# Optimization experiments

Measured on AMD Instinct MI355X. Metric: run time of the kernel, lower is better.

## Reference

```python
import jax, jax.numpy as jnp
import numpy as np

B, T, N_EMBD, N_HEAD = 2, 2048, 1024, 16
HEAD = N_EMBD // N_HEAD
WINDOW = 64


def setup_inputs() -> dict:
    key = jax.random.key(0)
    kq, kk, kv, kw = jax.random.split(key, 4)
    q = jax.random.normal(kq, (B, T, N_EMBD), dtype=jnp.float32)
    k = jax.random.normal(kk, (B, T, N_EMBD), dtype=jnp.float32)
    v = jax.random.normal(kv, (B, T, N_EMBD), dtype=jnp.float32)
    W_proj = jax.random.normal(kw, (N_EMBD, N_EMBD), dtype=jnp.float32) * (1.0 / np.sqrt(N_EMBD))
    b_proj = jnp.zeros((N_EMBD,), dtype=jnp.float32)
    return {"q": q, "k": k, "v": v, "W_proj": W_proj, "b_proj": b_proj}


def reference(q, k, v, W_proj, b_proj):
    Bsz, Tlen, _ = q.shape
    # split heads: [B, H, T, D]
    qh = q.reshape(Bsz, Tlen, N_HEAD, HEAD).transpose(0, 2, 1, 3)
    kh = k.reshape(Bsz, Tlen, N_HEAD, HEAD).transpose(0, 2, 1, 3)
    vh = v.reshape(Bsz, Tlen, N_HEAD, HEAD).transpose(0, 2, 1, 3)

    scale = 1.0 / np.sqrt(HEAD)
    scores = jnp.einsum('bhqd,bhkd->bhqk', qh, kh) * scale  # [B,H,T,T]

    # windowed additive mask: positions with |i-j| > WINDOW get -inf
    idx = jnp.arange(Tlen)
    dist = jnp.abs(idx[None, :] - idx[:, None])  # [T, T]
    scores = jnp.where(dist[None, None] > WINDOW, -jnp.inf, scores)

    attn = jax.nn.softmax(scores, axis=-1)
    y = jnp.einsum('bhqk,bhkd->bhqd', attn, vh)  # [B,H,T,D]
    y = y.transpose(0, 2, 1, 3).reshape(Bsz, Tlen, N_EMBD)
    return y @ W_proj.T + b_proj
```

## Files before the change

kernel.cpp:

```cpp
#include <hip/hip_runtime.h>
#include <hip/hip_bf16.h>

#define B_SZ 2
#define T_SZ 2048
#define NE   1024
#define NH   16
#define HD   64
#define WIN  64
#define QT   64
#define KT   192
#define GM   4096
#define GN   1024
#define GK   1024
#define KPAD 72
#define VPAD 200

__device__ ushort Wb_static[GN * GK];

__device__ __forceinline__ uint pack2(float lo, float hi) {
    uint r;
    asm("v_cvt_pk_bf16_f32 %0, %1, %2" : "=v"(r) : "v"(lo), "v"(hi));
    return r;
}
__device__ __forceinline__ uint4 pack8(float4 a, float4 b) {
    return make_uint4(pack2(a.x, a.y), pack2(a.z, a.w),
                      pack2(b.x, b.y), pack2(b.z, b.w));
}

typedef __attribute__((ext_vector_type(8))) short frag_ab;
typedef __attribute__((ext_vector_type(4))) float frag_cd;
union FragU { frag_ab f; uint u[4]; };

__global__ __launch_bounds__(256, 3) void attn_mfma_kernel(
    const float* __restrict__ q, const float* __restrict__ k,
    const float* __restrict__ v, const float* __restrict__ W,
    ushort* __restrict__ y)
{
    __shared__ __attribute__((aligned(16))) ushort pool[KT * KPAD + HD * VPAD];
    ushort* Ks = pool;
    ushort* Vt = pool + KT * KPAD;
    ushort* Ps = pool;

    const int bid = blockIdx.x;
    const int swz = ((bid & 7) << 7) | (bid >> 3);
    const int qs  = (swz & 31) * QT;
    const int h   = (swz >> 5) & 15;
    const int b   = swz >> 9;
    const int t   = threadIdx.x;
    const int kstart = qs - WIN;

    const int wv   = t >> 6;
    const int L    = t & 63;
    const int r16  = L & 15;
    const int quad = L >> 4;

    float4 qf0, qf1, qg0, qg1;
    {
        const float* qrow = q + ((size_t)(b * T_SZ + qs + wv * 16 + r16)) * NE + h * HD;
        const float4* p0 = (const float4*)(qrow + quad * 8);
        const float4* p1 = (const float4*)(qrow + 32 + quad * 8);
        qf0 = p0[0]; qf1 = p0[1]; qg0 = p1[0]; qg1 = p1[1];
    }

    {
        const int idx = bid * 256 + t;
        const float4 f = ((const float4*)W)[idx];
        ((uint2*)Wb_static)[idx] = make_uint2(pack2(f.x, f.y), pack2(f.z, f.w));
    }

#pragma unroll
    for (int i = 0; i < 6; ++i) {
        const int c  = t + 256 * i;
        const int j  = c >> 3;
        const int cc = c & 7;
        const int d8 = cc * 8;
        const int jg = kstart + j;
        const int jc = min(max(jg, 0), T_SZ - 1);
        const size_t off = ((size_t)(b * T_SZ + jc)) * NE + h * HD + d8;
        const float4* kp = (const float4*)(k + off);
        const float4* vp = (const float4*)(v + off);
        const float4 k0 = kp[0], k1 = kp[1];
        const float4 v0 = vp[0], v1 = vp[1];
        *(uint4*)&Ks[j * KPAD + d8] = pack8(k0, k1);
        ushort* vtc = &Vt[d8 * VPAD + (((j >> 3) ^ cc) * 8 + (j & 7))];
        const uint p01 = pack2(v0.x, v0.y);
        const uint p23 = pack2(v0.z, v0.w);
        const uint p45 = pack2(v1.x, v1.y);
        const uint p67 = pack2(v1.z, v1.w);
        vtc[0 * VPAD] = (ushort)p01; vtc[1 * VPAD] = (ushort)(p01 >> 16);
        vtc[2 * VPAD] = (ushort)p23; vtc[3 * VPAD] = (ushort)(p23 >> 16);
        vtc[4 * VPAD] = (ushort)p45; vtc[5 * VPAD] = (ushort)(p45 >> 16);
        vtc[6 * VPAD] = (ushort)p67; vtc[7 * VPAD] = (ushort)(p67 >> 16);
    }

    const float QSC = 0.125f * 1.44269504f;
    frag_ab aq0, aq1;
    {
        FragU u0, u1;
        u0.u[0] = pack2(qf0.x * QSC, qf0.y * QSC);
        u0.u[1] = pack2(qf0.z * QSC, qf0.w * QSC);
        u0.u[2] = pack2(qf1.x * QSC, qf1.y * QSC);
        u0.u[3] = pack2(qf1.z * QSC, qf1.w * QSC);
        u1.u[0] = pack2(qg0.x * QSC, qg0.y * QSC);
        u1.u[1] = pack2(qg0.z * QSC, qg0.w * QSC);
        u1.u[2] = pack2(qg1.x * QSC, qg1.y * QSC);
        u1.u[3] = pack2(qg1.z * QSC, qg1.w * QSC);
        aq0 = u0.f; aq1 = u1.f;
    }
    __syncthreads();

    frag_cd sacc[12];
#pragma unroll
    for (int nb = 0; nb < 12; ++nb) sacc[nb] = (frag_cd){0,0,0,0};
    __builtin_amdgcn_s_setprio(1);
#pragma unroll
    for (int nb = 0; nb < 12; ++nb) {
        const frag_ab b0 = *(const frag_ab*)&Ks[(nb * 16 + r16) * KPAD + quad * 8];
        const frag_ab b1 = *(const frag_ab*)&Ks[(nb * 16 + r16) * KPAD + 32 + quad * 8];
        sacc[nb] = __builtin_amdgcn_mfma_f32_16x16x32_bf16(aq0, b0, sacc[nb], 0, 0, 0);
        sacc[nb] = __builtin_amdgcn_mfma_f32_16x16x32_bf16(aq1, b1, sacc[nb], 0, 0, 0);
    }
    __builtin_amdgcn_s_setprio(0);

    const int base_m = wv * 16 + quad * 4;
    float l[4] = {0.f, 0.f, 0.f, 0.f};
#pragma unroll
    for (int nb = 0; nb < 12; ++nb) {
        const int jl = nb * 16 + r16;
        const int jg = kstart + jl;
        const bool jg_ok = (jg >= 0) & (jg < T_SZ);
#pragma unroll
        for (int r = 0; r < 4; ++r) {
            const int mrow = base_m + r;
            const bool valid = jg_ok & ((uint)(jl - mrow) <= 2u * WIN);
            const float p = valid ? exp2f(sacc[nb][r]) : 0.0f;
            l[r] += p;
            sacc[nb][r] = p;
        }
    }
#pragma unroll
    for (int r = 0; r < 4; ++r) {
        l[r] += __shfl_xor(l[r], 1);
        l[r] += __shfl_xor(l[r], 2);
        l[r] += __shfl_xor(l[r], 4);
        l[r] += __shfl_xor(l[r], 8);
    }

    __syncthreads();
#pragma unroll
    for (int nb = 0; nb < 12; ++nb) {
        const int jl = nb * 16 + r16;
        const uint p01 = pack2(sacc[nb][0], sacc[nb][1]);
        const uint p23 = pack2(sacc[nb][2], sacc[nb][3]);
        Ps[(base_m + 0) * VPAD + jl] = (ushort)p01;
        Ps[(base_m + 1) * VPAD + jl] = (ushort)(p01 >> 16);
        Ps[(base_m + 2) * VPAD + jl] = (ushort)p23;
        Ps[(base_m + 3) * VPAD + jl] = (ushort)(p23 >> 16);
    }
    __syncthreads();

    frag_ab ap[6];
#pragma unroll
    for (int kb = 0; kb < 6; ++kb)
        ap[kb] = *(const frag_ab*)&Ps[(wv * 16 + r16) * VPAD + kb * 32 + quad * 8];

    frag_cd oacc[4];
#pragma unroll
    for (int nb = 0; nb < 4; ++nb) oacc[nb] = (frag_cd){0,0,0,0};
    __builtin_amdgcn_s_setprio(1);
#pragma unroll
    for (int nb = 0; nb < 4; ++nb) {
        const int dr  = nb * 16 + r16;
        const int dsw = (dr >> 3) & 7;
#pragma unroll
        for (int kb = 0; kb < 6; ++kb) {
            const frag_ab bv = *(const frag_ab*)&Vt[dr * VPAD + (((kb * 4 + quad) ^ dsw) * 8)];
            oacc[nb] = __builtin_amdgcn_mfma_f32_16x16x32_bf16(ap[kb], bv, oacc[nb], 0, 0, 0);
        }
    }
    __builtin_amdgcn_s_setprio(0);

    float inv[4];
#pragma unroll
    for (int r = 0; r < 4; ++r) inv[r] = 1.0f / l[r];
#pragma unroll
    for (int nb = 0; nb < 4; ++nb) {
        const int d  = nb * 16 + r16;
        const uint p01 = pack2(oacc[nb][0] * inv[0], oacc[nb][1] * inv[1]);
        const uint p23 = pack2(oacc[nb][2] * inv[2], oacc[nb][3] * inv[3]);
        const size_t rb = (size_t)(b * T_SZ + qs + base_m) * NE + h * HD + d;
        y[rb + 0 * NE] = (ushort)p01;
        y[rb + 1 * NE] = (ushort)(p01 >> 16);
        y[rb + 2 * NE] = (ushort)p23;
        y[rb + 3 * NE] = (ushort)(p23 >> 16);
    }
}

__global__ __launch_bounds__(256, 2) void proj_gemm_kernel(
    const ushort* __restrict__ A,
    const float* __restrict__ bias, float* __restrict__ C)
{
    __shared__ __attribute__((aligned(16))) ushort As[128 * 128];
    __shared__ __attribute__((aligned(16))) ushort Bs[64 * 128];

    const ushort* Bw = Wb_static;
    const int t   = threadIdx.x;
    const int bid = blockIdx.x;
    const int swz = ((bid & 7) << 6) | (bid >> 3);
    const int tile_n = swz & 15;
    const int tile_m = swz >> 4;
    const int lane   = t & 63;
    const int wv     = t >> 6;
    const int wm     = wv >> 1;
    const int wn     = wv & 1;
    const int r16    = lane & 15;
    const int quad   = lane >> 4;

    frag_cd acc[4][2];
#pragma unroll
    for (int mi = 0; mi < 4; ++mi)
#pragma unroll
        for (int ni = 0; ni < 2; ++ni)
            acc[mi][ni] = (frag_cd){0.0f, 0.0f, 0.0f, 0.0f};

    const int fm = wm * 64 + r16;
    const int fn = wn * 32 + r16;
    const int sw = r16 & 7;

    for (int k0 = 0; k0 < GK; k0 += 128) {
#pragma unroll
        for (int i = 0; i < 8; ++i) {
            const int c   = t + 256 * i;
            const int row = c >> 4;
            const int src = ((c & 15) ^ (row & 7)) * 8;
            __builtin_amdgcn_global_load_lds(
                (const __attribute__((address_space(1))) unsigned int*)
                    (A + (size_t)(tile_m * 128 + row) * GK + k0 + src),
                (__attribute__((address_space(3))) unsigned int*)(As + c * 8), 16, 0, 0);
        }
#pragma unroll
        for (int i = 0; i < 4; ++i) {
            const int c   = t + 256 * i;
            const int row = c >> 4;
            const int src = ((c & 15) ^ (row & 7)) * 8;
            __builtin_amdgcn_global_load_lds(
                (const __attribute__((address_space(1))) unsigned int*)
                    (Bw + (size_t)(tile_n * 64 + row) * GK + k0 + src),
                (__attribute__((address_space(3))) unsigned int*)(Bs + c * 8), 16, 0, 0);
        }
        __syncthreads();

#pragma unroll
        for (int ks = 0; ks < 4; ++ks) {
            const int cidx = (((ks * 4) + quad) ^ sw) * 8;
            frag_ab af[4], bfr[2];
#pragma unroll
            for (int mi = 0; mi < 4; ++mi)
                af[mi] = *(const frag_ab*)&As[(fm + mi * 16) * 128 + cidx];
#pragma unroll
            for (int ni = 0; ni < 2; ++ni)
                bfr[ni] = *(const frag_ab*)&Bs[(fn + ni * 16) * 128 + cidx];
#pragma unroll
            for (int mi = 0; mi < 4; ++mi)
#pragma unroll
                for (int ni = 0; ni < 2; ++ni)
                    acc[mi][ni] = __builtin_amdgcn_mfma_f32_16x16x32_bf16(
                        af[mi], bfr[ni], acc[mi][ni], 0, 0, 0);
        }

        __syncthreads();
    }

#pragma unroll
    for (int mi = 0; mi < 4; ++mi) {
#pragma unroll
        for (int ni = 0; ni < 2; ++ni) {
            const int rbase = tile_m * 128 + wm * 64 + mi * 16 + quad * 4;
            const int cg    = tile_n * 64 + wn * 32 + ni * 16 + r16;
            const float bv  = bias[cg];
#pragma unroll
            for (int r = 0; r < 4; ++r)
                C[(size_t)(rbase + r) * GN + cg] = acc[mi][ni][r] + bv;
        }
    }
}

extern "C" void kernel_launch(void* const* d_in, const int* in_sizes, int n_in,
                              void* d_out, int out_size, void* d_ws, size_t ws_size,
                              hipStream_t stream) {
    (void)in_sizes; (void)n_in; (void)out_size; (void)ws_size;
    const float* q    = (const float*)d_in[0];
    const float* k    = (const float*)d_in[1];
    const float* v    = (const float*)d_in[2];
    const float* W    = (const float*)d_in[3];
    const float* bias = (const float*)d_in[4];
    float*  out = (float*)d_out;
    ushort* y   = (ushort*)d_ws;

    dim3 g1(1024);
    attn_mfma_kernel<<<g1, 256, 0, stream>>>(q, k, v, W, y);

    dim3 g2(512);
    proj_gemm_kernel<<<g2, 256, 0, stream>>>(y, bias, out);
}
```

Before: 118.9 us.

## Double-buffer projection GEMM LDS tiles and defer V transpose in attention

The projection GEMM now uses two 64-wide K tiles in LDS and issues the global-to-LDS load for the next tile before computing on the current one. The goal is to overlap memory latency with MFMA work. In the attention kernel, V is loaded into registers early but written transposed into LDS only after the QK/softmax phase, and __syncthreads is replaced with an lgkmcnt wait plus barrier. This raises register pressure from holding 12 float4 values. The GEMM's global_load_lds into buffer 1 is never waited on by vmcnt before the barrier, so correctness depends on the compiler inserting that wait, which is a race risk.

Measured after the change: 120.7 us. About the same (+1.5%).

```diff
diff --git a/kernel.cpp b/kernel.cpp
--- a/kernel.cpp
+++ b/kernel.cpp
@@ -31,6 +31,12 @@
 typedef __attribute__((ext_vector_type(4))) float frag_cd;
 union FragU { frag_ab f; uint u[4]; };
 
+#define LDS_BAR() do {                                        \
+    asm volatile("s_waitcnt lgkmcnt(0)" ::: "memory");        \
+    __builtin_amdgcn_s_barrier();                             \
+    asm volatile("" ::: "memory");                            \
+} while (0)
+
 __global__ __launch_bounds__(256, 3) void attn_mfma_kernel(
     const float* __restrict__ q, const float* __restrict__ k,
     const float* __restrict__ v, const float* __restrict__ W,
@@ -68,6 +74,7 @@
         ((uint2*)Wb_static)[idx] = make_uint2(pack2(f.x, f.y), pack2(f.z, f.w));
     }
 
+    float4 va[6], vb[6];
 #pragma unroll
     for (int i = 0; i < 6; ++i) {
         const int c  = t + 256 * i;
@@ -79,18 +86,9 @@
         const size_t off = ((size_t)(b * T_SZ + jc)) * NE + h * HD + d8;
         const float4* kp = (const float4*)(k + off);
         const float4* vp = (const float4*)(v + off);
+        va[i] = vp[0]; vb[i] = vp[1];
         const float4 k0 = kp[0], k1 = kp[1];
-        const float4 v0 = vp[0], v1 = vp[1];
         *(uint4*)&Ks[j * KPAD + d8] = pack8(k0, k1);
-        ushort* vtc = &Vt[d8 * VPAD + (((j >> 3) ^ cc) * 8 + (j & 7))];
-        const uint p01 = pack2(v0.x, v0.y);
-        const uint p23 = pack2(v0.z, v0.w);
-        const uint p45 = pack2(v1.x, v1.y);
-        const uint p67 = pack2(v1.z, v1.w);
-        vtc[0 * VPAD] = (ushort)p01; vtc[1 * VPAD] = (ushort)(p01 >> 16);
-        vtc[2 * VPAD] = (ushort)p23; vtc[3 * VPAD] = (ushort)(p23 >> 16);
-        vtc[4 * VPAD] = (ushort)p45; vtc[5 * VPAD] = (ushort)(p45 >> 16);
-        vtc[6 * VPAD] = (ushort)p67; vtc[7 * VPAD] = (ushort)(p67 >> 16);
     }
 
     const float QSC = 0.125f * 1.44269504f;
@@ -107,7 +105,7 @@
         u1.u[3] = pack2(qg1.z * QSC, qg1.w * QSC);
         aq0 = u0.f; aq1 = u1.f;
     }
-    __syncthreads();
+    LDS_BAR();
 
     frag_cd sacc[12];
 #pragma unroll
@@ -146,7 +144,24 @@
         l[r] += __shfl_xor(l[r], 8);
     }
 
-    __syncthreads();
+#pragma unroll
+    for (int i = 0; i < 6; ++i) {
+        const int c  = t + 256 * i;
+        const int j  = c >> 3;
+        const int cc = c & 7;
+        const int d8 = cc * 8;
+        ushort* vtc = &Vt[d8 * VPAD + (((j >> 3) ^ cc) * 8 + (j & 7))];
+        const uint p01 = pack2(va[i].x, va[i].y);
+        const uint p23 = pack2(va[i].z, va[i].w);
+        const uint p45 = pack2(vb[i].x, vb[i].y);
+        const uint p67 = pack2(vb[i].z, vb[i].w);
+        vtc[0 * VPAD] = (ushort)p01; vtc[1 * VPAD] = (ushort)(p01 >> 16);
+        vtc[2 * VPAD] = (ushort)p23; vtc[3 * VPAD] = (ushort)(p23 >> 16);
+        vtc[4 * VPAD] = (ushort)p45; vtc[5 * VPAD] = (ushort)(p45 >> 16);
+        vtc[6 * VPAD] = (ushort)p67; vtc[7 * VPAD] = (ushort)(p67 >> 16);
+    }
+
+    LDS_BAR();
 #pragma unroll
     for (int nb = 0; nb < 12; ++nb) {
         const int jl = nb * 16 + r16;
@@ -157,7 +172,7 @@
         Ps[(base_m + 2) * VPAD + jl] = (ushort)p23;
         Ps[(base_m + 3) * VPAD + jl] = (ushort)(p23 >> 16);
     }
-    __syncthreads();
+    LDS_BAR();
 
     frag_ab ap[6];
 #pragma unroll
@@ -196,12 +211,15 @@
     }
 }
 
+#define ASZ (128 * 64)
+#define BSZ (64 * 64)
+
 __global__ __launch_bounds__(256, 2) void proj_gemm_kernel(
     const ushort* __restrict__ A,
     const float* __restrict__ bias, float* __restrict__ C)
 {
-    __shared__ __attribute__((aligned(16))) ushort As[128 * 128];
-    __shared__ __attribute__((aligned(16))) ushort Bs[64 * 128];
+    __shared__ __attribute__((aligned(16))) ushort As[2 * ASZ];
+    __shared__ __attribute__((aligned(16))) ushort Bs[2 * BSZ];
 
     const ushort* Bw = Wb_static;
     const int t   = threadIdx.x;
@@ -227,47 +245,64 @@
     const int fn = wn * 32 + r16;
     const int sw = r16 & 7;
 
+#define STAGE_AB(buf, kk)                                                      \
+    {                                                                          \
+        _Pragma("unroll")                                                      \
+        for (int i = 0; i < 4; ++i) {                                          \
+            const int c   = t + 256 * i;                                       \
+            const int row = c >> 3;                                            \
+            const int src = ((c & 7) ^ (row & 7)) * 8;                         \
+            __builtin_amdgcn_global_load_lds(                                  \
+                (const __attribute__((address_space(1))) unsigned int*)        \
+                    (A + (size_t)(tile_m * 128 + row) * GK + (kk) + src),      \
+                (__attribute__((address_space(3))) unsigned int*)              \
+                    (As + (buf) * ASZ + c * 8), 16, 0, 0);                     \
+        }                                                                      \
+        _Pragma("unroll")                                                      \
+        for (int i = 0; i < 2; ++i) {                                          \
+            const int c   = t + 256 * i;                                       \
+            const int row = c >> 3;                                            \
+            const int src = ((c & 7) ^ (row & 7)) * 8;                         \
+            __builtin_amdgcn_global_load_lds(                                  \
+                (const __attribute__((address_space(1))) unsigned int*)        \
+                    (Bw + (size_t)(tile_n * 64 + row) * GK + (kk) + src),      \
+                (__attribute__((address_space(3))) unsigned int*)              \
+                    (Bs + (buf) * BSZ + c * 8), 16, 0, 0);                     \
+        }                                                                      \
+    }
+
+#define COMPUTE_AB(buf)                                                        \
+    {                                                                          \
+        _Pragma("unroll")                                                      \
+        for (int ks = 0; ks < 2; ++ks) {                                       \
+            const int cidx = (((ks * 4) + quad) ^ sw) * 8;                     \
+            frag_ab af[4], bfr[2];                                             \
+            _Pragma("unroll")                                                  \
+            for (int mi = 0; mi < 4; ++mi)                                     \
+                af[mi] = *(const frag_ab*)                                     \
+                    &As[(buf) * ASZ + (fm + mi * 16) * 64 + cidx];             \
+            _Pragma("unroll")                                                  \
+            for (int ni = 0; ni < 2; ++ni)                                     \
+                bfr[ni] = *(const frag_ab*)                                    \
+                    &Bs[(buf) * BSZ + (fn + ni * 16) * 64 + cidx];             \
+            _Pragma("unroll")                                                  \
+            for (int mi = 0; mi < 4; ++mi)                                     \
+                _Pragma("unroll")                                              \
+                for (int ni = 0; ni < 2; ++ni)                                 \
+                    acc[mi][ni] = __builtin_amdgcn_mfma_f32_16x16x32_bf16(     \
+                        af[mi], bfr[ni], acc[mi][ni], 0, 0, 0);                \
+        }                                                                      \
+    }
+
+    STAGE_AB(0, 0);
+    __syncthreads();
+
     for (int k0 = 0; k0 < GK; k0 += 128) {
-#pragma unroll
-        for (int i = 0; i < 8; ++i) {
-            const int c   = t + 256 * i;
-            const int row = c >> 4;
-            const int src = ((c & 15) ^ (row & 7)) * 8;
-            __builtin_amdgcn_global_load_lds(
-                (const __attribute__((address_space(1))) unsigned int*)
-                    (A + (size_t)(tile_m * 128 + row) * GK + k0 + src),
-                (__attribute__((address_space(3))) unsigned int*)(As + c * 8), 16, 0, 0);
-        }
-#pragma unroll
-        for (int i = 0; i < 4; ++i) {
-            const int c   = t + 256 * i;
-            const int row = c >> 4;
-            const int src = ((c & 15) ^ (row & 7)) * 8;
-            __builtin_amdgcn_global_load_lds(
-                (const __attribute__((address_space(1))) unsigned int*)
-                    (Bw + (size_t)(tile_n * 64 + row) * GK + k0 + src),
-                (__attribute__((address_space(3))) unsigned int*)(Bs + c * 8), 16, 0, 0);
-        }
+        STAGE_AB(1, k0 + 64);
+        COMPUTE_AB(0);
         __syncthreads();
-
-#pragma unroll
-        for (int ks = 0; ks < 4; ++ks) {
-            const int cidx = (((ks * 4) + quad) ^ sw) * 8;
-            frag_ab af[4], bfr[2];
-#pragma unroll
-            for (int mi = 0; mi < 4; ++mi)
-                af[mi] = *(const frag_ab*)&As[(fm + mi * 16) * 128 + cidx];
-#pragma unroll
-            for (int ni = 0; ni < 2; ++ni)
-                bfr[ni] = *(const frag_ab*)&Bs[(fn + ni * 16) * 128 + cidx];
-#pragma unroll
-            for (int mi = 0; mi < 4; ++mi)
-#pragma unroll
-                for (int ni = 0; ni < 2; ++ni)
-                    acc[mi][ni] = __builtin_amdgcn_mfma_f32_16x16x32_bf16(
-                        af[mi], bfr[ni], acc[mi][ni], 0, 0, 0);
-        }
-
+        if (k0 + 128 < GK) STAGE_AB(0, k0 + 128);
+        COMPUTE_AB(1);
         __syncthreads();
     }
 
```
